# Performance work log

Hardware: AMD Instinct MI355X
Metric: run time of the kernel (lower is better)

The kernel has to match this reference:

```python
import jax, jax.numpy as jnp
import numpy as np

N_NODES = 100000
N_EDGES = 1600000
IN_CH = 128
HEADS = 4
HID = 32
OUT_CH = 128
NEG_SLOPE = 0.2


def setup_inputs() -> dict:
    key = jax.random.key(0)
    ks = jax.random.split(key, 7)
    sc = 1.0 / np.sqrt(IN_CH)
    return {
        "x": jax.random.normal(ks[0], (N_NODES, IN_CH), dtype=jnp.float32),
        "edge_index": jax.random.randint(ks[1], (2, N_EDGES), 0, N_NODES, dtype=jnp.int32),
        "W": jax.random.normal(ks[2], (IN_CH, HEADS * HID), dtype=jnp.float32) * sc,
        "att_src": jax.random.normal(ks[3], (HEADS, HID), dtype=jnp.float32) * sc,
        "att_dst": jax.random.normal(ks[4], (HEADS, HID), dtype=jnp.float32) * sc,
        "lin_w": jax.random.normal(ks[5], (HEADS * HID, OUT_CH), dtype=jnp.float32) * (1.0 / np.sqrt(HEADS * HID)),
        "lin_b": jax.random.normal(ks[6], (OUT_CH,), dtype=jnp.float32) * 0.01,
    }


def reference(x, edge_index, W, att_src, att_dst, lin_w, lin_b):
    N = x.shape[0]
    src, dst = edge_index[0], edge_index[1]
    # node-wise linear transform -> [N, H, C]
    h = (x @ W).reshape(N, HEADS, HID)
    # per-node attention logit components [N, H]
    a_src = jnp.einsum("nhc,hc->nh", h, att_src)
    a_dst = jnp.einsum("nhc,hc->nh", h, att_dst)
    # per-edge logits with LeakyReLU [E, H]
    e = jax.nn.leaky_relu(a_src[src] + a_dst[dst], negative_slope=NEG_SLOPE)
    # segment softmax over destination neighborhoods
    m = jax.ops.segment_max(e, dst, num_segments=N)
    ex = jnp.exp(e - m[dst])
    s = jax.ops.segment_sum(ex, dst, num_segments=N)
    alpha = ex / (s[dst] + 1e-16)
    # weighted scatter-sum of source features [N, H, C] -> concat heads
    msg = h[src] * alpha[:, :, None]
    out = jax.ops.segment_sum(msg, dst, num_segments=N).reshape(N, HEADS * HID)
    # trailing dense + ReLU
    return jax.nn.relu(out @ lin_w + lin_b)
```

## Files before the change

### kernel.cpp

```cpp
#include <hip/hip_runtime.h>
#include <hip/hip_fp16.h>

#define NB   256
#define NBLK 256
#define BSH  9

typedef _Float16 f16;
typedef _Float16 half8 __attribute__((ext_vector_type(8)));
typedef float f32x4 __attribute__((ext_vector_type(4)));


__global__ __launch_bounds__(256) void k_gemm_att(
    const float* __restrict__ A, const float* __restrict__ B,
    const float* __restrict__ att_s, const float* __restrict__ att_d,
    f16* __restrict__ Hh, float* __restrict__ as_out, float* __restrict__ ad_out,
    int M)
{
    __shared__ __align__(16) f16 as_lds[64 * 136];
    __shared__ __align__(16) f16 bs_lds[128 * 136];
    int t = threadIdx.x;
    int row0 = blockIdx.x * 64;

    {
        int r = t >> 2;
        int kq = (t & 3) * 32;
        const float* ap = A + (size_t)(row0 + r) * 128 + kq;
        bool valid = (row0 + r) < M;
        f16* dst = as_lds + r * 136 + kq;
#pragma unroll
        for (int j = 0; j < 8; ++j) {
            float4 v = valid ? *(const float4*)(ap + j * 4) : make_float4(0.f, 0.f, 0.f, 0.f);
            dst[j * 4 + 0] = (f16)v.x; dst[j * 4 + 1] = (f16)v.y;
            dst[j * 4 + 2] = (f16)v.z; dst[j * 4 + 3] = (f16)v.w;
        }
    }
    {
        int k = t >> 1;
        int n0 = (t & 1) * 64;
        const float* bp = B + (size_t)k * 128 + n0;
#pragma unroll
        for (int j = 0; j < 16; ++j) {
            float4 v = *(const float4*)(bp + j * 4);
            bs_lds[(n0 + j * 4 + 0) * 136 + k] = (f16)v.x;
            bs_lds[(n0 + j * 4 + 1) * 136 + k] = (f16)v.y;
            bs_lds[(n0 + j * 4 + 2) * 136 + k] = (f16)v.z;
            bs_lds[(n0 + j * 4 + 3) * 136 + k] = (f16)v.w;
        }
    }
    __syncthreads();

    int w = t >> 6, ln = t & 63;
    int rr = (w & 1) * 32;
    int cc = (w >> 1) * 64;
    int q = ln >> 4, m = ln & 15;

    f32x4 acc[2][4];
#pragma unroll
    for (int i = 0; i < 2; ++i)
#pragma unroll
        for (int j = 0; j < 4; ++j) acc[i][j] = (f32x4){0.f, 0.f, 0.f, 0.f};

#pragma unroll
    for (int ks = 0; ks < 4; ++ks) {
        int k0 = ks * 32 + q * 8;
        half8 a0 = *(const half8*)(as_lds + (rr + m) * 136 + k0);
        half8 a1 = *(const half8*)(as_lds + (rr + 16 + m) * 136 + k0);
        half8 bf[4];
#pragma unroll
        for (int j = 0; j < 4; ++j)
            bf[j] = *(const half8*)(bs_lds + (cc + j * 16 + m) * 136 + k0);
#pragma unroll
        for (int j = 0; j < 4; ++j) {
            acc[0][j] = __builtin_amdgcn_mfma_f32_16x16x32_f16(a0, bf[j], acc[0][j], 0, 0, 0);
            acc[1][j] = __builtin_amdgcn_mfma_f32_16x16x32_f16(a1, bf[j], acc[1][j], 0, 0, 0);
        }
    }
    __syncthreads();
#pragma unroll
    for (int i = 0; i < 2; ++i)
#pragma unroll
        for (int j = 0; j < 4; ++j)
#pragma unroll
            for (int g = 0; g < 4; ++g)
                as_lds[(rr + i * 16 + q * 4 + g) * 136 + cc + j * 16 + m] = (f16)acc[i][j][g];
    __syncthreads();
    {
        int r = t >> 2, cq = (t & 3) * 32;
        if (row0 + r < M) {
            float4 o0 = *(const float4*)(as_lds + r * 136 + cq);
            float4 o1 = *(const float4*)(as_lds + r * 136 + cq + 8);
            float4 o2 = *(const float4*)(as_lds + r * 136 + cq + 16);
            float4 o3 = *(const float4*)(as_lds + r * 136 + cq + 24);
            float4* hp = (float4*)(Hh + (size_t)(row0 + r) * 128 + cq);
            hp[0] = o0; hp[1] = o1; hp[2] = o2; hp[3] = o3;
        }
    }
    {
        int rl = w * 16 + m;
        int head = q;
        float ds = 0.f, dd = 0.f;
#pragma unroll
        for (int ch = 0; ch < 4; ++ch) {
            half8 hv = *(const half8*)(as_lds + rl * 136 + head * 32 + ch * 8);
            float4 s0 = *(const float4*)(att_s + head * 32 + ch * 8);
            float4 s1 = *(const float4*)(att_s + head * 32 + ch * 8 + 4);
            float4 d0 = *(const float4*)(att_d + head * 32 + ch * 8);
            float4 d1 = *(const float4*)(att_d + head * 32 + ch * 8 + 4);
            ds += (float)hv[0] * s0.x + (float)hv[1] * s0.y + (float)hv[2] * s0.z + (float)hv[3] * s0.w
                + (float)hv[4] * s1.x + (float)hv[5] * s1.y + (float)hv[6] * s1.z + (float)hv[7] * s1.w;
            dd += (float)hv[0] * d0.x + (float)hv[1] * d0.y + (float)hv[2] * d0.z + (float)hv[3] * d0.w
                + (float)hv[4] * d1.x + (float)hv[5] * d1.y + (float)hv[6] * d1.z + (float)hv[7] * d1.w;
        }
        if (row0 + rl < M) {
            as_out[(row0 + rl) * 4 + head] = ds;
            ad_out[(row0 + rl) * 4 + head] = dd;
        }
    }
}


__global__ __launch_bounds__(256) void k_gemm_bias_relu(
    const f16* __restrict__ Ah, const float* __restrict__ B,
    const float* __restrict__ bias, float* __restrict__ Out, int M)
{
    __shared__ __align__(16) f16 as_lds[64 * 136];
    __shared__ __align__(16) f16 bs_lds[128 * 136];
    int t = threadIdx.x;
    int row0 = blockIdx.x * 64;

    {
        int r = t >> 2;
        int kq = (t & 3) * 32;
        f16* dst = as_lds + r * 136 + kq;
        if (row0 + r < M) {
            const float4* ap = (const float4*)(Ah + (size_t)(row0 + r) * 128 + kq);
#pragma unroll
            for (int j = 0; j < 4; ++j) *(float4*)(dst + j * 8) = ap[j];
        } else {
#pragma unroll
            for (int j = 0; j < 32; ++j) dst[j] = (f16)0.f;
        }
    }
    {
        int k = t >> 1;
        int n0 = (t & 1) * 64;
        const float* bp = B + (size_t)k * 128 + n0;
#pragma unroll
        for (int j = 0; j < 16; ++j) {
            float4 v = *(const float4*)(bp + j * 4);
            bs_lds[(n0 + j * 4 + 0) * 136 + k] = (f16)v.x;
            bs_lds[(n0 + j * 4 + 1) * 136 + k] = (f16)v.y;
            bs_lds[(n0 + j * 4 + 2) * 136 + k] = (f16)v.z;
            bs_lds[(n0 + j * 4 + 3) * 136 + k] = (f16)v.w;
        }
    }
    __syncthreads();

    int w = t >> 6, ln = t & 63;
    int rr = (w & 1) * 32;
    int cc = (w >> 1) * 64;
    int q = ln >> 4, m = ln & 15;

    f32x4 acc[2][4];
#pragma unroll
    for (int i = 0; i < 2; ++i)
#pragma unroll
        for (int j = 0; j < 4; ++j) acc[i][j] = (f32x4){0.f, 0.f, 0.f, 0.f};

#pragma unroll
    for (int ks = 0; ks < 4; ++ks) {
        int k0 = ks * 32 + q * 8;
        half8 a0 = *(const half8*)(as_lds + (rr + m) * 136 + k0);
        half8 a1 = *(const half8*)(as_lds + (rr + 16 + m) * 136 + k0);
        half8 bf[4];
#pragma unroll
        for (int j = 0; j < 4; ++j)
            bf[j] = *(const half8*)(bs_lds + (cc + j * 16 + m) * 136 + k0);
#pragma unroll
        for (int j = 0; j < 4; ++j) {
            acc[0][j] = __builtin_amdgcn_mfma_f32_16x16x32_f16(a0, bf[j], acc[0][j], 0, 0, 0);
            acc[1][j] = __builtin_amdgcn_mfma_f32_16x16x32_f16(a1, bf[j], acc[1][j], 0, 0, 0);
        }
    }
    float bv[4];
#pragma unroll
    for (int j = 0; j < 4; ++j) bv[j] = bias[cc + j * 16 + m];
#pragma unroll
    for (int i = 0; i < 2; ++i)
#pragma unroll
        for (int g = 0; g < 4; ++g) {
            int row = row0 + rr + i * 16 + q * 4 + g;
            if (row < M) {
#pragma unroll
                for (int j = 0; j < 4; ++j)
                    Out[(size_t)row * 128 + cc + j * 16 + m] = fmaxf(acc[i][j][g] + bv[j], 0.f);
            }
        }
}


__global__ __launch_bounds__(256) void k_ph_hist(
    const int* __restrict__ dst, int* __restrict__ bh, int E, int chunk)
{
    __shared__ int hist[NB];
    int t = threadIdx.x;
    hist[t] = 0;
    __syncthreads();
    int e0 = blockIdx.x * chunk;
    int e1 = min(e0 + chunk, E);
    for (int e = e0 + t; e < e1; e += 256)
        atomicAdd(&hist[dst[e] >> BSH], 1);
    __syncthreads();
    bh[t * NBLK + blockIdx.x] = hist[t];
}

__global__ __launch_bounds__(1024) void k_ph_scan(int* __restrict__ bh)
{
    __shared__ int sd[1024];
    const int per = (NB * NBLK) / 1024;
    int t = threadIdx.x;
    int base = t * per;
    int loc[per];
    int sum = 0;
#pragma unroll
    for (int j = 0; j < per; ++j) { loc[j] = bh[base + j]; sum += loc[j]; }
    sd[t] = sum;
    __syncthreads();
    for (int o = 1; o < 1024; o <<= 1) {
        int x = (t >= o) ? sd[t - o] : 0;
        __syncthreads();
        sd[t] += x;
        __syncthreads();
    }
    int run = sd[t] - sum;
#pragma unroll
    for (int j = 0; j < per; ++j) { bh[base + j] = run; run += loc[j]; }
}

__global__ __launch_bounds__(256) void k_ph_bin(
    const int* __restrict__ ei, const int* __restrict__ bh,
    int2* __restrict__ binned, int E, int chunk)
{
    __shared__ int boff[NB];
    int t = threadIdx.x;
    boff[t] = bh[t * NBLK + blockIdx.x];
    __syncthreads();
    int e0 = blockIdx.x * chunk;
    int e1 = min(e0 + chunk, E);
    for (int e = e0 + t; e < e1; e += 256) {
        int s = ei[e];
        int d = ei[E + e];
        int p = atomicAdd(&boff[d >> BSH], 1);
        binned[p] = make_int2(s, d);
    }
}

__global__ __launch_bounds__(256) void k_ph_csr(
    const int2* __restrict__ binned, const int* __restrict__ bh,
    int* __restrict__ csr, int* __restrict__ off, int* __restrict__ deg,
    int N, int E)
{
    __shared__ int cnt[512], loff[512], sd[256];
    int b = blockIdx.x;
    int lo = b << BSH;
    if (lo >= N) return;
    int t = threadIdx.x;
    int seg = bh[b * NBLK];
    int segend = (b + 1 < NB) ? bh[(b + 1) * NBLK] : E;
    int len = segend - seg;
    cnt[t] = 0; cnt[t + 256] = 0;
    __syncthreads();
    for (int i = t; i < len; i += 256)
        atomicAdd(&cnt[binned[seg + i].y - lo], 1);
    __syncthreads();
    int a0 = cnt[2 * t], a1 = cnt[2 * t + 1];
    int s = a0 + a1;
    sd[t] = s;
    __syncthreads();
    for (int o = 1; o < 256; o <<= 1) {
        int x = (t >= o) ? sd[t - o] : 0;
        __syncthreads();
        sd[t] += x;
        __syncthreads();
    }
    int ex = sd[t] - s;
    loff[2 * t] = ex;
    loff[2 * t + 1] = ex + a0;
    int n0 = lo + 2 * t;
    if (n0 < N)     { off[n0] = seg + ex;          deg[n0] = a0; }
    if (n0 + 1 < N) { off[n0 + 1] = seg + ex + a0; deg[n0 + 1] = a1; }
    __syncthreads();
    for (int i = t; i < len; i += 256) {
        int2 e = binned[seg + i];
        int p = atomicAdd(&loff[e.y - lo], 1);
        csr[seg + p] = e.x;
    }
}


__global__ __launch_bounds__(256) void k_gather(
    const __half* __restrict__ Hh, const float* __restrict__ as_,
    const float* __restrict__ ad_, const int* __restrict__ off,
    const int* __restrict__ deg, const int* __restrict__ csr,
    __half* __restrict__ P, int N)
{
    __shared__ float ex_s[4][256];
    __shared__ int src_s[4][64];
    int wid = threadIdx.x >> 6;
    int lane = threadIdx.x & 63;
    int n = blockIdx.x * 4 + wid;
    if (n >= N) return;
    int dg = deg[n];
    int base = off[n];
    float4 adn = *(const float4*)(ad_ + (size_t)n * 4);
    int g = lane >> 4;
    int li = lane & 15;
    int hh = li >> 2;
    float s0 = 0.f, s1 = 0.f, s2 = 0.f, s3 = 0.f;
    float acc[8] = {0.f, 0.f, 0.f, 0.f, 0.f, 0.f, 0.f, 0.f};

    for (int c0 = 0; c0 < dg; c0 += 64) {
        int cnt = min(64, dg - c0);
        if (lane < cnt) {
            int se = csr[base + c0 + lane];
            float4 as = *(const float4*)(as_ + (size_t)se * 4);
            float e0 = as.x + adn.x, e1 = as.y + adn.y;
            float e2 = as.z + adn.z, e3 = as.w + adn.w;
            e0 = fmaxf(e0, 0.2f * e0); e1 = fmaxf(e1, 0.2f * e1);
            e2 = fmaxf(e2, 0.2f * e2); e3 = fmaxf(e3, 0.2f * e3);
            float x0 = __expf(e0), x1 = __expf(e1);
            float x2 = __expf(e2), x3 = __expf(e3);
            s0 += x0; s1 += x1; s2 += x2; s3 += x3;
            *(float4*)&ex_s[wid][lane * 4] = make_float4(x0, x1, x2, x3);
            src_s[wid][lane] = se;
        }
        __asm__ volatile("s_waitcnt lgkmcnt(0)" ::: "memory");
        int iters = (cnt + 3) >> 2;
        for (int ii = 0; ii < iters; ++ii) {
            int j = ii * 4 + g;
            bool valid = j < cnt;
            float w = valid ? ex_s[wid][j * 4 + hh] : 0.f;
            int se = valid ? src_s[wid][j] : 0;
            float4 raw = *(const float4*)(Hh + (size_t)se * 128 + li * 8);
            __half2* ph = (__half2*)&raw;
            float2 f0 = __half22float2(ph[0]);
            float2 f1 = __half22float2(ph[1]);
            float2 f2 = __half22float2(ph[2]);
            float2 f3 = __half22float2(ph[3]);
            acc[0] = fmaf(w, f0.x, acc[0]);
            acc[1] = fmaf(w, f0.y, acc[1]);
            acc[2] = fmaf(w, f1.x, acc[2]);
            acc[3] = fmaf(w, f1.y, acc[3]);
            acc[4] = fmaf(w, f2.x, acc[4]);
            acc[5] = fmaf(w, f2.y, acc[5]);
            acc[6] = fmaf(w, f3.x, acc[6]);
            acc[7] = fmaf(w, f3.y, acc[7]);
        }
        __asm__ volatile("s_waitcnt lgkmcnt(0)" ::: "memory");
    }

#pragma unroll
    for (int o = 1; o < 64; o <<= 1) {
        s0 += __shfl_xor(s0, o);
        s1 += __shfl_xor(s1, o);
        s2 += __shfl_xor(s2, o);
        s3 += __shfl_xor(s3, o);
    }
#pragma unroll
    for (int o = 16; o < 64; o <<= 1)
#pragma unroll
        for (int c = 0; c < 8; ++c) acc[c] += __shfl_xor(acc[c], o);

    float sh = (hh == 0) ? s0 : (hh == 1) ? s1 : (hh == 2) ? s2 : s3;
    float inv = 1.f / (sh + 1e-16f);
    if (g == 0) {
        __half2 o4[4];
#pragma unroll
        for (int k = 0; k < 4; ++k)
            o4[k] = __float22half2_rn(make_float2(acc[2 * k] * inv, acc[2 * k + 1] * inv));
        *(float4*)(P + (size_t)n * 128 + li * 8) = *(float4*)o4;
    }
}


extern "C" void kernel_launch(void* const* d_in, const int* in_sizes, int n_in,
                              void* d_out, int out_size, void* d_ws, size_t ws_size,
                              hipStream_t stream)
{
    const float* x     = (const float*)d_in[0];
    const int*   ei    = (const int*)d_in[1];
    const float* W     = (const float*)d_in[2];
    const float* att_s = (const float*)d_in[3];
    const float* att_d = (const float*)d_in[4];
    const float* lin_w = (const float*)d_in[5];
    const float* lin_b = (const float*)d_in[6];
    float* out = (float*)d_out;
    int N = in_sizes[0] / 128;
    int E = in_sizes[1] / 2;

    char* p = (char*)d_ws;
    auto alloc = [&](size_t bytes) { char* r = p; p += (bytes + 255) & ~(size_t)255; return r; };
    f16*    Hh   = (f16*)alloc((size_t)N * 128 * 2);
    f16*    P    = (f16*)alloc((size_t)N * 128 * 2);
    float*  AS   = (float*)alloc((size_t)N * 4 * 4);
    float*  AD   = (float*)alloc((size_t)N * 4 * 4);
    int*    deg  = (int*)alloc((size_t)N * 4);
    int*    off  = (int*)alloc((size_t)N * 4);
    int*    csr  = (int*)alloc((size_t)E * 4);
    int2*   binned = (int2*)alloc((size_t)E * 8);
    int*    bh   = (int*)alloc((size_t)NB * NBLK * 4);

    int chunk = (E + NBLK - 1) / NBLK;
    int mb = (N + 63) / 64;
    k_gemm_att<<<mb, 256, 0, stream>>>(x, W, att_s, att_d, Hh, AS, AD, N);
    k_ph_hist<<<NBLK, 256, 0, stream>>>(ei + E, bh, E, chunk);
    k_ph_scan<<<1, 1024, 0, stream>>>(bh);
    k_ph_bin<<<NBLK, 256, 0, stream>>>(ei, bh, binned, E, chunk);
    k_ph_csr<<<NB, 256, 0, stream>>>(binned, bh, csr, off, deg, N, E);
    k_gather<<<(N + 3) / 4, 256, 0, stream>>>((const __half*)Hh, AS, AD, off, deg, csr, (__half*)P, N);
    k_gemm_bias_relu<<<mb, 256, 0, stream>>>(P, lin_w, lin_b, out, N);
}
```

Before: 304.7 us.

## Pre-transpose weights to fp16, pack binned edges, use half2 FMA in gather

```diff
diff --git a/kernel.cpp b/kernel.cpp
--- a/kernel.cpp
+++ b/kernel.cpp
@@ -7,45 +7,43 @@
 
 typedef _Float16 f16;
 typedef _Float16 half8 __attribute__((ext_vector_type(8)));
+typedef __fp16 pk16x2 __attribute__((ext_vector_type(2)));
 typedef float f32x4 __attribute__((ext_vector_type(4)));
 
+__global__ void k_prep(const float* __restrict__ W, const float* __restrict__ LW,
+                       f16* __restrict__ Wt, f16* __restrict__ LWt)
+{
+    int n = blockIdx.x & 127;
+    const float* src = (blockIdx.x < 128) ? W : LW;
+    f16* dst = (blockIdx.x < 128) ? Wt : LWt;
+    int k = threadIdx.x;
+    dst[n * 128 + k] = (f16)src[k * 128 + n];
+}
 
 __global__ __launch_bounds__(256) void k_gemm_att(
-    const float* __restrict__ A, const float* __restrict__ B,
+    const float* __restrict__ A, const f16* __restrict__ Wt,
     const float* __restrict__ att_s, const float* __restrict__ att_d,
     f16* __restrict__ Hh, float* __restrict__ as_out, float* __restrict__ ad_out,
     int M)
 {
     __shared__ __align__(16) f16 as_lds[64 * 136];
-    __shared__ __align__(16) f16 bs_lds[128 * 136];
     int t = threadIdx.x;
     int row0 = blockIdx.x * 64;
 
     {
-        int r = t >> 2;
-        int kq = (t & 3) * 32;
+        int r = t >> 2, kq = (t & 3) * 32;
         const float* ap = A + (size_t)(row0 + r) * 128 + kq;
         bool valid = (row0 + r) < M;
-        f16* dst = as_lds + r * 136 + kq;
+        pk16x2 hb[16];
 #pragma unroll
         for (int j = 0; j < 8; ++j) {
             float4 v = valid ? *(const float4*)(ap + j * 4) : make_float4(0.f, 0.f, 0.f, 0.f);
-            dst[j * 4 + 0] = (f16)v.x; dst[j * 4 + 1] = (f16)v.y;
-            dst[j * 4 + 2] = (f16)v.z; dst[j * 4 + 3] = (f16)v.w;
-        }
-    }
-    {
-        int k = t >> 1;
-        int n0 = (t & 1) * 64;
-        const float* bp = B + (size_t)k * 128 + n0;
-#pragma unroll
-        for (int j = 0; j < 16; ++j) {
-            float4 v = *(const float4*)(bp + j * 4);
-            bs_lds[(n0 + j * 4 + 0) * 136 + k] = (f16)v.x;
-            bs_lds[(n0 + j * 4 + 1) * 136 + k] = (f16)v.y;
-            bs_lds[(n0 + j * 4 + 2) * 136 + k] = (f16)v.z;
-            bs_lds[(n0 + j * 4 + 3) * 136 + k] = (f16)v.w;
-        }
+            hb[2 * j]     = __builtin_amdgcn_cvt_pkrtz(v.x, v.y);
+            hb[2 * j + 1] = __builtin_amdgcn_cvt_pkrtz(v.z, v.w);
+        }
+        f16* dst = as_lds + r * 136 + kq;
+#pragma unroll
+        for (int j = 0; j < 4; ++j) *(float4*)(dst + j * 8) = ((float4*)hb)[j];
     }
     __syncthreads();
 
@@ -60,6 +58,7 @@
 #pragma unroll
         for (int j = 0; j < 4; ++j) acc[i][j] = (f32x4){0.f, 0.f, 0.f, 0.f};
 
+    const f16* wp = Wt + (size_t)(cc + m) * 128 + q * 8;
 #pragma unroll
     for (int ks = 0; ks < 4; ++ks) {
         int k0 = ks * 32 + q * 8;
@@ -68,7 +67,7 @@
         half8 bf[4];
 #pragma unroll
         for (int j = 0; j < 4; ++j)
-            bf[j] = *(const half8*)(bs_lds + (cc + j * 16 + m) * 136 + k0);
+            bf[j] = *(const half8*)(wp + j * 16 * 128 + ks * 32);
 #pragma unroll
         for (int j = 0; j < 4; ++j) {
             acc[0][j] = __builtin_amdgcn_mfma_f32_16x16x32_f16(a0, bf[j], acc[0][j], 0, 0, 0);
@@ -118,40 +117,24 @@
     }
 }
 
-
 __global__ __launch_bounds__(256) void k_gemm_bias_relu(
-    const f16* __restrict__ Ah, const float* __restrict__ B,
+    const f16* __restrict__ Ah, const f16* __restrict__ LWt,
     const float* __restrict__ bias, float* __restrict__ Out, int M)
 {
     __shared__ __align__(16) f16 as_lds[64 * 136];
-    __shared__ __align__(16) f16 bs_lds[128 * 136];
     int t = threadIdx.x;
     int row0 = blockIdx.x * 64;
-
     {
-        int r = t >> 2;
-        int kq = (t & 3) * 32;
+        int r = t >> 2, kq = (t & 3) * 32;
         f16* dst = as_lds + r * 136 + kq;
         if (row0 + r < M) {
             const float4* ap = (const float4*)(Ah + (size_t)(row0 + r) * 128 + kq);
 #pragma unroll
             for (int j = 0; j < 4; ++j) *(float4*)(dst + j * 8) = ap[j];
         } else {
-#pragma unroll
-            for (int j = 0; j < 32; ++j) dst[j] = (f16)0.f;
-        }
-    }
-    {
-        int k = t >> 1;
-        int n0 = (t & 1) * 64;
-        const float* bp = B + (size_t)k * 128 + n0;
-#pragma unroll
-        for (int j = 0; j < 16; ++j) {
-            float4 v = *(const float4*)(bp + j * 4);
-            bs_lds[(n0 + j * 4 + 0) * 136 + k] = (f16)v.x;
-            bs_lds[(n0 + j * 4 + 1) * 136 + k] = (f16)v.y;
-            bs_lds[(n0 + j * 4 + 2) * 136 + k] = (f16)v.z;
-            bs_lds[(n0 + j * 4 + 3) * 136 + k] = (f16)v.w;
+            float4 z = make_float4(0.f, 0.f, 0.f, 0.f);
+#pragma unroll
+            for (int j = 0; j < 4; ++j) *(float4*)(dst + j * 8) = z;
         }
     }
     __syncthreads();
@@ -167,6 +150,7 @@
 #pragma unroll
         for (int j = 0; j < 4; ++j) acc[i][j] = (f32x4){0.f, 0.f, 0.f, 0.f};
 
+    const f16* wp = LWt + (size_t)(cc + m) * 128 + q * 8;
 #pragma unroll
     for (int ks = 0; ks < 4; ++ks) {
         int k0 = ks * 32 + q * 8;
@@ -175,7 +159,7 @@
         half8 bf[4];
 #pragma unroll
         for (int j = 0; j < 4; ++j)
-            bf[j] = *(const half8*)(bs_lds + (cc + j * 16 + m) * 136 + k0);
+            bf[j] = *(const half8*)(wp + j * 16 * 128 + ks * 32);
 #pragma unroll
         for (int j = 0; j < 4; ++j) {
             acc[0][j] = __builtin_amdgcn_mfma_f32_16x16x32_f16(a0, bf[j], acc[0][j], 0, 0, 0);
@@ -239,7 +223,7 @@
 
 __global__ __launch_bounds__(256) void k_ph_bin(
     const int* __restrict__ ei, const int* __restrict__ bh,
-    int2* __restrict__ binned, int E, int chunk)
+    int* __restrict__ binned, int E, int chunk)
 {
     __shared__ int boff[NB];
     int t = threadIdx.x;
@@ -251,12 +235,12 @@
         int s = ei[e];
         int d = ei[E + e];
         int p = atomicAdd(&boff[d >> BSH], 1);
-        binned[p] = make_int2(s, d);
+        binned[p] = s | ((d & ((1 << BSH) - 1)) << 17);
     }
 }
 
 __global__ __launch_bounds__(256) void k_ph_csr(
-    const int2* __restrict__ binned, const int* __restrict__ bh,
+    const int* __restrict__ binned, const int* __restrict__ bh,
     int* __restrict__ csr, int* __restrict__ off, int* __restrict__ deg,
     int N, int E)
 {
@@ -271,7 +255,7 @@
     cnt[t] = 0; cnt[t + 256] = 0;
     __syncthreads();
     for (int i = t; i < len; i += 256)
-        atomicAdd(&cnt[binned[seg + i].y - lo], 1);
+        atomicAdd(&cnt[(unsigned)binned[seg + i] >> 17], 1);
     __syncthreads();
     int a0 = cnt[2 * t], a1 = cnt[2 * t + 1];
     int s = a0 + a1;
@@ -291,12 +275,11 @@
     if (n0 + 1 < N) { off[n0 + 1] = seg + ex + a0; deg[n0 + 1] = a1; }
     __syncthreads();
     for (int i = t; i < len; i += 256) {
-        int2 e = binned[seg + i];
-        int p = atomicAdd(&loff[e.y - lo], 1);
-        csr[seg + p] = e.x;
-    }
-}
-
+        int v = binned[seg + i];
+        int p = atomicAdd(&loff[(unsigned)v >> 17], 1);
+        csr[seg + p] = v & 0x1ffff;
+    }
+}
 
 __global__ __launch_bounds__(256) void k_gather(
     const __half* __restrict__ Hh, const float* __restrict__ as_,
@@ -304,7 +287,7 @@
     const int* __restrict__ deg, const int* __restrict__ csr,
     __half* __restrict__ P, int N)
 {
-    __shared__ float ex_s[4][256];
+    __shared__ __half2 exh[4][4][68];
     __shared__ int src_s[4][64];
     int wid = threadIdx.x >> 6;
     int lane = threadIdx.x & 63;
@@ -321,8 +304,9 @@
 
     for (int c0 = 0; c0 < dg; c0 += 64) {
         int cnt = min(64, dg - c0);
-        if (lane < cnt) {
-            int se = csr[base + c0 + lane];
+        {
+            int idx = c0 + lane;
+            int se = csr[base + min(idx, dg - 1)];
             float4 as = *(const float4*)(as_ + (size_t)se * 4);
             float e0 = as.x + adn.x, e1 = as.y + adn.y;
             float e2 = as.z + adn.z, e3 = as.w + adn.w;
@@ -330,31 +314,41 @@
             e2 = fmaxf(e2, 0.2f * e2); e3 = fmaxf(e3, 0.2f * e3);
             float x0 = __expf(e0), x1 = __expf(e1);
             float x2 = __expf(e2), x3 = __expf(e3);
+            if (idx >= dg) { x0 = x1 = x2 = x3 = 0.f; }
             s0 += x0; s1 += x1; s2 += x2; s3 += x3;
-            *(float4*)&ex_s[wid][lane * 4] = make_float4(x0, x1, x2, x3);
+            exh[wid][0][lane] = __float2half2_rn(x0);
+            exh[wid][1][lane] = __float2half2_rn(x1);
+            exh[wid][2][lane] = __float2half2_rn(x2);
+            exh[wid][3][lane] = __float2half2_rn(x3);
             src_s[wid][lane] = se;
         }
         __asm__ volatile("s_waitcnt lgkmcnt(0)" ::: "memory");
         int iters = (cnt + 3) >> 2;
+        __half2 ah[4];
+        ah[0] = ah[1] = ah[2] = ah[3] = __float2half2_rn(0.f);
         for (int ii = 0; ii < iters; ++ii) {
             int j = ii * 4 + g;
-            bool valid = j < cnt;
-            float w = valid ? ex_s[wid][j * 4 + hh] : 0.f;
-            int se = valid ? src_s[wid][j] : 0;
+            __half2 w2 = exh[wid][hh][j];
+            int se = src_s[wid][j];
             float4 raw = *(const float4*)(Hh + (size_t)se * 128 + li * 8);
             __half2* ph = (__half2*)&raw;
-            float2 f0 = __half22float2(ph[0]);
-            float2 f1 = __half22float2(ph[1]);
-            float2 f2 = __half22float2(ph[2]);
-            float2 f3 = __half22float2(ph[3]);
-            acc[0] = fmaf(w, f0.x, acc[0]);
-            acc[1] = fmaf(w, f0.y, acc[1]);
-            acc[2] = fmaf(w, f1.x, acc[2]);
-            acc[3] = fmaf(w, f1.y, acc[3]);
-            acc[4] = fmaf(w, f2.x, acc[4]);
-            acc[5] = fmaf(w, f2.y, acc[5]);
-            acc[6] = fmaf(w, f3.x, acc[6]);
-            acc[7] = fmaf(w, f3.y, acc[7]);
+            ah[0] = __hfma2(ph[0], w2, ah[0]);
+            ah[1] = __hfma2(ph[1], w2, ah[1]);
+            ah[2] = __hfma2(ph[2], w2, ah[2]);
+            ah[3] = __hfma2(ph[3], w2, ah[3]);
+            if ((ii & 7) == 7) {
+#pragma unroll
+                for (int k = 0; k < 4; ++k) {
+                    float2 f = __half22float2(ah[k]);
+                    acc[2 * k] += f.x; acc[2 * k + 1] += f.y;
+                    ah[k] = __float2half2_rn(0.f);
+                }
+            }
+        }
+#pragma unroll
+        for (int k = 0; k < 4; ++k) {
+            float2 f = __half22float2(ah[k]);
+            acc[2 * k] += f.x; acc[2 * k + 1] += f.y;
         }
         __asm__ volatile("s_waitcnt lgkmcnt(0)" ::: "memory");
     }
@@ -402,21 +396,24 @@
     auto alloc = [&](size_t bytes) { char* r = p; p += (bytes + 255) & ~(size_t)255; return r; };
     f16*    Hh   = (f16*)alloc((size_t)N * 128 * 2);
     f16*    P    = (f16*)alloc((size_t)N * 128 * 2);
+    f16*    Wt   = (f16*)alloc(128 * 128 * 2);
+    f16*    LWt  = (f16*)alloc(128 * 128 * 2);
     float*  AS   = (float*)alloc((size_t)N * 4 * 4);
     float*  AD   = (float*)alloc((size_t)N * 4 * 4);
     int*    deg  = (int*)alloc((size_t)N * 4);
     int*    off  = (int*)alloc((size_t)N * 4);
     int*    csr  = (int*)alloc((size_t)E * 4);
-    int2*   binned = (int2*)alloc((size_t)E * 8);
+    int*    binned = (int*)alloc((size_t)E * 4);
     int*    bh   = (int*)alloc((size_t)NB * NBLK * 4);
 
     int chunk = (E + NBLK - 1) / NBLK;
     int mb = (N + 63) / 64;
-    k_gemm_att<<<mb, 256, 0, stream>>>(x, W, att_s, att_d, Hh, AS, AD, N);
+    k_prep<<<256, 128, 0, stream>>>(W, lin_w, Wt, LWt);
+    k_gemm_att<<<mb, 256, 0, stream>>>(x, Wt, att_s, att_d, Hh, AS, AD, N);
     k_ph_hist<<<NBLK, 256, 0, stream>>>(ei + E, bh, E, chunk);
     k_ph_scan<<<1, 1024, 0, stream>>>(bh);
     k_ph_bin<<<NBLK, 256, 0, stream>>>(ei, bh, binned, E, chunk);
     k_ph_csr<<<NB, 256, 0, stream>>>(binned, bh, csr, off, deg, N, E);
     k_gather<<<(N + 3) / 4, 256, 0, stream>>>((const __half*)Hh, AS, AD, off, deg, csr, (__half*)P, N);
-    k_gemm_bias_relu<<<mb, 256, 0, stream>>>(P, lin_w, lin_b, out, N);
-}
+    k_gemm_bias_relu<<<mb, 256, 0, stream>>>(P, LWt, lin_b, out, N);
+}
```

After: 303.9 us. About the same (-0.2%).
